# Optimization experiments

Measured on AMD Instinct MI355X. Metric: run time of the kernel, lower is better.

Reference implementation:

```python
import jax, jax.numpy as jnp
import numpy as np

N = 100000
E = 1000000
IN_C, HID, OUT_C = 128, 128, 40
DROPOUT_P = 0.5
BN_EPS = 1e-5


def setup_inputs() -> dict:
    key = jax.random.key(0)
    ks = jax.random.split(key, 10)
    x = jax.random.normal(ks[0], (N, IN_C), dtype=jnp.float32)
    edge_index = jax.random.randint(ks[1], (2, E), 0, N, dtype=jnp.int32)

    def glorot(k, fan_in, fan_out):
        lim = np.sqrt(6.0 / (fan_in + fan_out)).astype(np.float32)
        return jax.random.uniform(k, (fan_in, fan_out), jnp.float32, -lim, lim)

    return {
        "x": x,
        "edge_index": edge_index,
        "W1": glorot(ks[2], IN_C, HID), "b1": jnp.zeros((HID,), jnp.float32),
        "g1": jnp.ones((HID,), jnp.float32), "be1": jnp.zeros((HID,), jnp.float32),
        "W2": glorot(ks[3], HID, HID), "b2": jnp.zeros((HID,), jnp.float32),
        "g2": jnp.ones((HID,), jnp.float32), "be2": jnp.zeros((HID,), jnp.float32),
        "W3": glorot(ks[4], HID, OUT_C), "b3": jnp.zeros((OUT_C,), jnp.float32),
    }


def _deg_inv_sqrt(dst):
    # degree from destination nodes, +1 for the added self loop (PyG gcn_norm)
    deg = jax.ops.segment_sum(jnp.ones((E,), jnp.float32), dst, num_segments=N) + 1.0
    return jax.lax.rsqrt(deg)


def _gcn_conv(h, W, b, src, dst, dinv):
    # h: [N, Cin] -> [N, Cout]; y = D^-1/2 (A + I) D^-1/2 (h W) + b
    hw = h @ W
    norm = dinv[src] * dinv[dst]                      # [E]
    msg = hw[src] * norm[:, None]                     # [E, Cout] gather (memory-bound)
    agg = jax.ops.segment_sum(msg, dst, num_segments=N)
    agg = agg + hw * (dinv * dinv)[:, None]           # self-loop contribution
    return agg + b


def _batchnorm(h, gamma, beta):
    mu = jnp.mean(h, axis=0)
    var = jnp.mean(jnp.square(h - mu), axis=0)        # biased, training mode
    return (h - mu) * jax.lax.rsqrt(var + BN_EPS) * gamma + beta


def _dropout(h, key):
    keep = jax.random.bernoulli(key, 1.0 - DROPOUT_P, h.shape)
    return jnp.where(keep, h / (1.0 - DROPOUT_P), 0.0)


def reference(x, edge_index, W1, b1, g1, be1, W2, b2, g2, be2, W3, b3):
    src, dst = edge_index[0], edge_index[1]
    dinv = _deg_inv_sqrt(dst)
    dk = jax.random.split(jax.random.key(42), 2)

    h = _gcn_conv(x, W1, b1, src, dst, dinv)
    h = _dropout(jax.nn.relu(_batchnorm(h, g1, be1)), dk[0])

    h = _gcn_conv(h, W2, b2, src, dst, dinv)
    h = _dropout(jax.nn.relu(_batchnorm(h, g2, be2)), dk[1])

    h = _gcn_conv(h, W3, b3, src, dst, dinv)
    return jax.nn.log_softmax(h, axis=1)
```

## Files before the change

### kernel.cpp

```cpp
#include <hip/hip_runtime.h>
#include <math.h>

typedef __attribute__((ext_vector_type(8))) short bf16x8;
typedef __attribute__((ext_vector_type(4))) float f32x4;

__device__ __forceinline__ float bfbits2f(unsigned short b){
  return __uint_as_float(((unsigned)b) << 16);
}
__device__ __forceinline__ unsigned short f2bfbits(float f){
  unsigned u = __float_as_uint(f);
  unsigned r = u + 0x7fffu + ((u >> 16) & 1u);
  return (unsigned short)(r >> 16);
}

__device__ __forceinline__ uint4 ld16(const void* __restrict__ base, unsigned byteoff){
  return *(const uint4*)((const char*)base + byteoff);
}
__device__ __forceinline__ uint2 ld8(const void* __restrict__ base, unsigned byteoff){
  return *(const uint2*)((const char*)base + byteoff);
}

__host__ __device__ __forceinline__ unsigned rotl32(unsigned v, int d){
  return (v << d) | (v >> (32 - d));
}
__host__ __device__ __forceinline__ void tf2x32(unsigned k0, unsigned k1,
                                                unsigned c0, unsigned c1,
                                                unsigned &o0, unsigned &o1)
{
  unsigned ks2 = k0 ^ k1 ^ 0x1BD11BDAu;
  unsigned x0 = c0 + k0, x1 = c1 + k1;
#define TFR(r) x0 += x1; x1 = rotl32(x1, r); x1 ^= x0;
  TFR(13) TFR(15) TFR(26) TFR(6)
  x0 += k1;  x1 += ks2 + 1u;
  TFR(17) TFR(29) TFR(16) TFR(24)
  x0 += ks2; x1 += k0 + 2u;
  TFR(13) TFR(15) TFR(26) TFR(6)
  x0 += k0;  x1 += k1 + 3u;
  TFR(17) TFR(29) TFR(16) TFR(24)
  x0 += k1;  x1 += ks2 + 4u;
  TFR(13) TFR(15) TFR(26) TFR(6)
  x0 += ks2; x1 += k0 + 5u;
#undef TFR
  o0 = x0; o1 = x1;
}

__global__ __launch_bounds__(256) void k_countpos(const int* __restrict__ dst,
                                                  int* __restrict__ cnt,
                                                  int* __restrict__ pos, int E)
{
  int g = blockIdx.x * 256 + threadIdx.x;
  int base = g * 4;
  if (base + 3 < E){
    int4 d = ((const int4*)dst)[g];
    int4 p;
    p.x = atomicAdd(&cnt[d.x], 1);
    p.y = atomicAdd(&cnt[d.y], 1);
    p.z = atomicAdd(&cnt[d.z], 1);
    p.w = atomicAdd(&cnt[d.w], 1);
    ((int4*)pos)[g] = p;
  } else {
    for (int j = 0; j < 4; j++){
      int e = base + j;
      if (e < E) pos[e] = atomicAdd(&cnt[dst[e]], 1);
    }
  }
}

__global__ __launch_bounds__(256) void k_blocksum(const int* __restrict__ cnt,
                                                  int* __restrict__ bsum, int N)
{
  __shared__ int sh[256];
  int t = threadIdx.x;
  int base = blockIdx.x * 1024 + t * 4;
  int s = 0;
  #pragma unroll
  for (int j = 0; j < 4; j++){ int i = base + j; if (i < N) s += cnt[i]; }
  sh[t] = s; __syncthreads();
  for (int off = 128; off; off >>= 1){
    if (t < off) sh[t] += sh[t + off];
    __syncthreads();
  }
  if (t == 0) bsum[blockIdx.x] = sh[0];
}

__global__ __launch_bounds__(256) void k_scansums(const int* __restrict__ bsum,
                                                  int* __restrict__ boff,
                                                  int* __restrict__ rowstart,
                                                  int NB, int N)
{
  __shared__ int sh[256];
  int t = threadIdx.x;
  int v = (t < NB) ? bsum[t] : 0;
  sh[t] = v; __syncthreads();
  for (int off = 1; off < 256; off <<= 1){
    int x = sh[t];
    int y = (t >= off) ? sh[t - off] : 0;
    __syncthreads();
    sh[t] = x + y;
    __syncthreads();
  }
  if (t < NB) boff[t] = sh[t] - v;
  if (t == NB - 1) rowstart[N] = sh[t];
}

__global__ __launch_bounds__(256) void k_scanfinal(const int* __restrict__ cnt,
                                                   const int* __restrict__ boff,
                                                   int* __restrict__ rowstart,
                                                   float* __restrict__ dinv, int N)
{
  __shared__ int sh[256];
  int t = threadIdx.x;
  int base = blockIdx.x * 1024 + t * 4;
  int c0 = 0, c1 = 0, c2 = 0, c3 = 0;
  if (base + 0 < N) c0 = cnt[base + 0];
  if (base + 1 < N) c1 = cnt[base + 1];
  if (base + 2 < N) c2 = cnt[base + 2];
  if (base + 3 < N) c3 = cnt[base + 3];
  int s = c0 + c1 + c2 + c3;
  sh[t] = s; __syncthreads();
  for (int off = 1; off < 256; off <<= 1){
    int x = sh[t];
    int y = (t >= off) ? sh[t - off] : 0;
    __syncthreads();
    sh[t] = x + y;
    __syncthreads();
  }
  int excl = sh[t] - s + boff[blockIdx.x];
  if (base + 0 < N){ rowstart[base+0] = excl;          dinv[base+0] = rsqrtf((float)c0 + 1.f); }
  if (base + 1 < N){ rowstart[base+1] = excl+c0;       dinv[base+1] = rsqrtf((float)c1 + 1.f); }
  if (base + 2 < N){ rowstart[base+2] = excl+c0+c1;    dinv[base+2] = rsqrtf((float)c2 + 1.f); }
  if (base + 3 < N){ rowstart[base+3] = excl+c0+c1+c2; dinv[base+3] = rsqrtf((float)c3 + 1.f); }
}

__global__ __launch_bounds__(256) void k_fill(const int* __restrict__ src,
                                              const int* __restrict__ dst,
                                              const int* __restrict__ pos,
                                              const int* __restrict__ rowstart,
                                              int* __restrict__ csr, int E)
{
  int g = blockIdx.x * 256 + threadIdx.x;
  int base = g * 4;
  if (base + 3 < E){
    int4 d = ((const int4*)dst)[g];
    int4 p = ((const int4*)pos)[g];
    int4 s = ((const int4*)src)[g];
    int r0 = rowstart[d.x], r1 = rowstart[d.y], r2 = rowstart[d.z], r3 = rowstart[d.w];
    csr[r0 + p.x] = s.x;
    csr[r1 + p.y] = s.y;
    csr[r2 + p.z] = s.z;
    csr[r3 + p.w] = s.w;
  } else {
    for (int j = 0; j < 4; j++){
      int e = base + j;
      if (e < E) csr[rowstart[dst[e]] + pos[e]] = src[e];
    }
  }
}

__global__ __launch_bounds__(256) void k_wt(const float* __restrict__ W1,
                                            const float* __restrict__ W2,
                                            const float* __restrict__ W3,
                                            unsigned short* __restrict__ WT1,
                                            unsigned short* __restrict__ WT2,
                                            unsigned short* __restrict__ WT3)
{
  const float* W; unsigned short* WT; int Cout, Cpad;
  if (blockIdx.x == 0){ W = W1; WT = WT1; Cout = 128; Cpad = 128; }
  else if (blockIdx.x == 1){ W = W2; WT = WT2; Cout = 128; Cpad = 128; }
  else { W = W3; WT = WT3; Cout = 40; Cpad = 48; }
  int tot = Cpad * 128;
  for (int i = threadIdx.x; i < tot; i += 256){
    int n = i >> 7, k = i & 127;
    float v = (n < Cout) ? W[k * Cout + n] : 0.f;
    WT[i] = f2bfbits(v);
  }
}

template<int NT, int MODE, int MASKGEN>
__global__ __launch_bounds__(256) void k_gemm_mfma(const void* __restrict__ Ap,
                                                   const unsigned short* __restrict__ WT,
                                                   const float* __restrict__ dinv,
                                                   const float* __restrict__ stats,
                                                   const float* __restrict__ g,
                                                   const float* __restrict__ be,
                                                   const unsigned* __restrict__ mask,
                                                   unsigned* __restrict__ maskw,
                                                   unsigned wk0, unsigned wk1, int Mw,
                                                   float invN,
                                                   unsigned short* __restrict__ outb,
                                                   int N, int Cout, int Cstride)
{
  __shared__ uint4 Wl4[NT * 16 * 16];
  __shared__ float bnS[128], bnB[128];
  const int t = threadIdx.x;
  const int w = t >> 6, l = t & 63;
  const int lm = l & 15, q = l >> 4;
  const long rb0 = (long)blockIdx.x * 64;
  const int wrow0 = w * 16;
  const long grow = rb0 + wrow0 + lm;
  const bool inr = (grow < N);

  uint4 rawU[4];
  float4 rawF[4][2];
  uint4 mws;
  if (inr){
    #pragma unroll
    for (int kt = 0; kt < 4; kt++){
      int c = kt * 4 + q;
      if (MODE == 0){
        const float* ap = (const float*)Ap + grow * 128 + c * 8;
        rawF[kt][0] = *(const float4*)ap;
        rawF[kt][1] = *(const float4*)(ap + 4);
      } else {
        rawU[kt] = *(const uint4*)((const unsigned short*)Ap + grow * 128 + c * 8);
      }
    }
    if (MODE == 2) mws = *(const uint4*)(mask + ((unsigned)grow << 2));
  }

  {
    const uint4* s4 = (const uint4*)WT;
    const int tot = NT * 16 * 16;
    for (int i = t; i < tot; i += 256){
      int n = i >> 4, c = i & 15;
      Wl4[n * 16 + (c ^ (n & 15))] = s4[i];
    }
  }
  if (MODE == 2 && t < 128){
    float ss = 0.f, qq = 0.f;
    #pragma unroll
    for (int i = 0; i < 16; i++){
      ss += stats[i * 256 + t];
      qq += stats[i * 256 + 128 + t];
    }
    float mean = ss * invN;
    float var = fmaxf(qq * invN - mean * mean, 0.f);
    float rstd = rsqrtf(var + 1e-5f);
    float sc = g[t] * rstd;
    bnS[t] = sc;
    bnB[t] = be[t] - mean * sc;
  }
  __syncthreads();

  bf16x8 afr[4];
  #pragma unroll
  for (int kt = 0; kt < 4; kt++){
    uint4 chunk = make_uint4(0u, 0u, 0u, 0u);
    if (inr){
      if (MODE == 0){
        chunk.x = (unsigned)f2bfbits(rawF[kt][0].x) | ((unsigned)f2bfbits(rawF[kt][0].y) << 16);
        chunk.y = (unsigned)f2bfbits(rawF[kt][0].z) | ((unsigned)f2bfbits(rawF[kt][0].w) << 16);
        chunk.z = (unsigned)f2bfbits(rawF[kt][1].x) | ((unsigned)f2bfbits(rawF[kt][1].y) << 16);
        chunk.w = (unsigned)f2bfbits(rawF[kt][1].z) | ((unsigned)f2bfbits(rawF[kt][1].w) << 16);
      } else {
        int c = kt * 4 + q;
        unsigned mb = (&mws.x)[kt] >> (q * 8);
        const unsigned* rw = &rawU[kt].x;
        unsigned* cw = &chunk.x;
        #pragma unroll
        for (int h = 0; h < 4; h++){
          int ch = c * 8 + 2 * h;
          float f0 = bfbits2f((unsigned short)(rw[h] & 0xffffu));
          float f1 = bfbits2f((unsigned short)(rw[h] >> 16));
          f0 = fmaxf(fmaf(f0, bnS[ch],     bnB[ch]),     0.f);
          f1 = fmaxf(fmaf(f1, bnS[ch + 1], bnB[ch + 1]), 0.f);
          f0 = ((mb >> (2 * h))     & 1u) ? 0.f : f0 * 2.f;
          f1 = ((mb >> (2 * h + 1)) & 1u) ? 0.f : f1 * 2.f;
          cw[h] = (unsigned)f2bfbits(f0) | ((unsigned)f2bfbits(f1) << 16);
        }
      }
    }
    afr[kt] = *(bf16x8*)&chunk;
  }

  f32x4 acc[NT];
  #pragma unroll
  for (int nt = 0; nt < NT; nt++){
    acc[nt][0] = 0.f; acc[nt][1] = 0.f; acc[nt][2] = 0.f; acc[nt][3] = 0.f;
  }

  #pragma unroll
  for (int kt = 0; kt < 4; kt++){
    const int x = kt * 4 + q;
    #pragma unroll
    for (int nt = 0; nt < NT; nt++){
      int brow = nt * 16 + lm;
      bf16x8 b = *(const bf16x8*)&Wl4[brow * 16 + (x ^ (brow & 15))];
      acc[nt] = __builtin_amdgcn_mfma_f32_16x16x32_bf16(afr[kt], b, acc[nt], 0, 0, 0);
    }
  }

  #pragma unroll
  for (int r = 0; r < 4; r++){
    long row = rb0 + wrow0 + q * 4 + r;
    if (row < N){
      float dv = dinv[row];
      #pragma unroll
      for (int nt = 0; nt < NT; nt++){
        int col = nt * 16 + lm;
        if (col < Cout)
          outb[row * Cstride + col] = f2bfbits(acc[nt][r] * dv);
      }
    }
  }

  if (MASKGEN){
    int gg = blockIdx.x * 256 + t;
    if (gg < Mw){
      unsigned bits = 0u;
      #pragma unroll 4
      for (int j = 0; j < 32; j++){
        unsigned w0, w1;
        tf2x32(wk0, wk1, 0u, (unsigned)gg * 32u + (unsigned)j, w0, w1);
        bits |= (((w0 ^ w1) >> 31) << j);
      }
      maskw[gg] = bits;
    }
  }
}

#define ACC8(U) do{ uint4 _u = (U); \
  a0 += __uint_as_float(_u.x << 16); \
  a1 += __uint_as_float(_u.x & 0xffff0000u); \
  a2 += __uint_as_float(_u.y << 16); \
  a3 += __uint_as_float(_u.y & 0xffff0000u); \
  a4 += __uint_as_float(_u.z << 16); \
  a5 += __uint_as_float(_u.z & 0xffff0000u); \
  a6 += __uint_as_float(_u.w << 16); \
  a7 += __uint_as_float(_u.w & 0xffff0000u); }while(0)

__global__ __launch_bounds__(256) void k_agg128s(const unsigned short* __restrict__ hw,
                                                 const int* __restrict__ rs,
                                                 const int* __restrict__ csr,
                                                 const float* __restrict__ dinv,
                                                 unsigned short* __restrict__ outb,
                                                 float* __restrict__ stats,
                                                 int N)
{
  const int l = threadIdx.x;
  const int ns = l >> 4;
  const int sl = l & 15;
  const int ty = threadIdx.y;
  const int grp = ty * 4 + ns;
  const int base = blockIdx.x * 32;
  const unsigned slB = (unsigned)sl * 16u;

  float s0=0.f,s1=0.f,s2=0.f,s3=0.f,s4=0.f,s5=0.f,s6=0.f,s7=0.f;
  float q0=0.f,q1=0.f,q2=0.f,q3=0.f,q4=0.f,q5=0.f,q6=0.f,q7=0.f;

  #pragma unroll 1
  for (int it = 0; it < 2; it++){
    int v = base + it * 16 + grp;
    if (v < N){
      float a0=0.f,a1=0.f,a2=0.f,a3=0.f,a4=0.f,a5=0.f,a6=0.f,a7=0.f;
      ACC8(ld16(hw, (unsigned)v * 256u + slB));
      int e0 = rs[v], e1 = rs[v + 1];
      int i = e0;
      for (; i + 4 <= e1; i += 4){
        int sa = csr[i], sb = csr[i+1], sc = csr[i+2], sd = csr[i+3];
        uint4 m0 = ld16(hw, (unsigned)sa * 256u + slB);
        uint4 m1 = ld16(hw, (unsigned)sb * 256u + slB);
        uint4 m2 = ld16(hw, (unsigned)sc * 256u + slB);
        uint4 m3 = ld16(hw, (unsigned)sd * 256u + slB);
        ACC8(m0); ACC8(m1); ACC8(m2); ACC8(m3);
      }
      for (; i < e1; i++){
        ACC8(ld16(hw, (unsigned)csr[i] * 256u + slB));
      }
      float dv = dinv[v];
      a0*=dv; a1*=dv; a2*=dv; a3*=dv; a4*=dv; a5*=dv; a6*=dv; a7*=dv;
      uint4 o;
      o.x = (unsigned)f2bfbits(a0) | ((unsigned)f2bfbits(a1) << 16);
      o.y = (unsigned)f2bfbits(a2) | ((unsigned)f2bfbits(a3) << 16);
      o.z = (unsigned)f2bfbits(a4) | ((unsigned)f2bfbits(a5) << 16);
      o.w = (unsigned)f2bfbits(a6) | ((unsigned)f2bfbits(a7) << 16);
      *(uint4*)((char*)outb + (unsigned)v * 256u + slB) = o;
      s0+=a0; q0=fmaf(a0,a0,q0);  s1+=a1; q1=fmaf(a1,a1,q1);
      s2+=a2; q2=fmaf(a2,a2,q2);  s3+=a3; q3=fmaf(a3,a3,q3);
      s4+=a4; q4=fmaf(a4,a4,q4);  s5+=a5; q5=fmaf(a5,a5,q5);
      s6+=a6; q6=fmaf(a6,a6,q6);  s7+=a7; q7=fmaf(a7,a7,q7);
    }
  }

  __shared__ float shS[16][128], shQ[16][128];
  *(float4*)&shS[grp][sl * 8]     = make_float4(s0, s1, s2, s3);
  *(float4*)&shS[grp][sl * 8 + 4] = make_float4(s4, s5, s6, s7);
  *(float4*)&shQ[grp][sl * 8]     = make_float4(q0, q1, q2, q3);
  *(float4*)&shQ[grp][sl * 8 + 4] = make_float4(q4, q5, q6, q7);
  __syncthreads();
  int t = ty * 64 + threadIdx.x;
  if (t < 128){
    float ss = 0.f, qq = 0.f;
    #pragma unroll
    for (int g2 = 0; g2 < 16; g2++){ ss += shS[g2][t]; qq += shQ[g2][t]; }
    float* dstat = stats + (blockIdx.x & 15) * 256;
    atomicAdd(&dstat[t], ss);
    atomicAdd(&dstat[128 + t], qq);
  }
}

__global__ __launch_bounds__(256) void k_agg40lsm(const unsigned short* __restrict__ hw,
                                                  const int* __restrict__ rs,
                                                  const int* __restrict__ csr,
                                                  const float* __restrict__ dinv,
                                                  const float* __restrict__ b3,
                                                  float* __restrict__ out, int N)
{
  const int l = threadIdx.x;
  const int ns = l >> 4, sl = l & 15;
  const int v = blockIdx.x * 16 + threadIdx.y * 4 + ns;
  const bool act = (v < N) && (sl < 10);
  const unsigned slB = (unsigned)sl * 8u;
  float a0 = 0.f, a1 = 0.f, a2 = 0.f, a3 = 0.f, dv = 1.f;
  if (act){
    dv = dinv[v];
    uint2 u = ld8(hw, (unsigned)v * 128u + slB);
    a0 = __uint_as_float(u.x << 16);
    a1 = __uint_as_float(u.x & 0xffff0000u);
    a2 = __uint_as_float(u.y << 16);
    a3 = __uint_as_float(u.y & 0xffff0000u);
    int e0 = rs[v], e1 = rs[v + 1];
    int i = e0;
#define ACCU2(U) do{ uint2 _u = (U); \
    a0 += __uint_as_float(_u.x << 16); \
    a1 += __uint_as_float(_u.x & 0xffff0000u); \
    a2 += __uint_as_float(_u.y << 16); \
    a3 += __uint_as_float(_u.y & 0xffff0000u); }while(0)
    for (; i + 4 <= e1; i += 4){
      int sa = csr[i], sb = csr[i+1], sc = csr[i+2], sd = csr[i+3];
      uint2 m0 = ld8(hw, (unsigned)sa * 128u + slB);
      uint2 m1 = ld8(hw, (unsigned)sb * 128u + slB);
      uint2 m2 = ld8(hw, (unsigned)sc * 128u + slB);
      uint2 m3 = ld8(hw, (unsigned)sd * 128u + slB);
      ACCU2(m0); ACCU2(m1); ACCU2(m2); ACCU2(m3);
    }
    for (; i < e1; i++){
      ACCU2(ld8(hw, (unsigned)csr[i] * 128u + slB));
    }
#undef ACCU2
  }
  float x0 = act ? fmaf(a0, dv, b3[sl * 4 + 0]) : -INFINITY;
  float x1 = act ? fmaf(a1, dv, b3[sl * 4 + 1]) : -INFINITY;
  float x2 = act ? fmaf(a2, dv, b3[sl * 4 + 2]) : -INFINITY;
  float x3 = act ? fmaf(a3, dv, b3[sl * 4 + 3]) : -INFINITY;
  float m = fmaxf(fmaxf(x0, x1), fmaxf(x2, x3));
  #pragma unroll
  for (int off = 8; off; off >>= 1) m = fmaxf(m, __shfl_xor(m, off, 16));
  float e = act ? (expf(x0 - m) + expf(x1 - m) + expf(x2 - m) + expf(x3 - m)) : 0.f;
  #pragma unroll
  for (int off = 8; off; off >>= 1) e += __shfl_xor(e, off, 16);
  float lse = m + logf(e);
  if (act){
    float4 o;
    o.x = x0 - lse; o.y = x1 - lse; o.z = x2 - lse; o.w = x3 - lse;
    *reinterpret_cast<float4*>(out + (size_t)v * 40 + sl * 4) = o;
  }
}

extern "C" void kernel_launch(void* const* d_in, const int* in_sizes, int n_in,
                              void* d_out, int out_size, void* d_ws, size_t ws_size,
                              hipStream_t stream)
{
  const float* x  = (const float*)d_in[0];
  const int* ei   = (const int*)d_in[1];
  const float* W1 = (const float*)d_in[2];
  const float* g1 = (const float*)d_in[4];
  const float* be1= (const float*)d_in[5];
  const float* W2 = (const float*)d_in[6];
  const float* g2 = (const float*)d_in[8];
  const float* be2= (const float*)d_in[9];
  const float* W3 = (const float*)d_in[10];
  const float* b3 = (const float*)d_in[11];
  float* out = (float*)d_out;

  const int N = in_sizes[0] / 128;
  const int E = in_sizes[1] / 2;
  const int* srcv = ei;
  const int* dstv = ei + E;

  char* ws = (char*)d_ws;
  size_t off = 0;
  auto take = [&](size_t bytes) -> void* {
    void* p = ws + off;
    off = (off + bytes + 255) & ~(size_t)255;
    return p;
  };
  int*   cnt      = (int*)  take((size_t)N * 4);
  int*   pos      = (int*)  take((size_t)E * 4);
  int*   rowstart = (int*)  take((size_t)(N + 1) * 4);
  int*   csr      = (int*)  take((size_t)E * 4);
  float* dinv     = (float*)take((size_t)N * 4);
  int*   bsum     = (int*)  take(256 * 4);
  int*   boff     = (int*)  take(256 * 4);
  float* stats1   = (float*)take(2 * 16 * 256 * 4);
  float* stats2   = stats1 + 16 * 256;
  unsigned* mask1 = (unsigned*)take((size_t)N * 4 * 4);
  unsigned* mask2 = (unsigned*)take((size_t)N * 4 * 4);
  unsigned short* WT1 = (unsigned short*)take(128 * 128 * 2);
  unsigned short* WT2 = (unsigned short*)take(128 * 128 * 2);
  unsigned short* WT3 = (unsigned short*)take(48 * 128 * 2);
  unsigned short* bufX = (unsigned short*)take((size_t)N * 128 * 2);
  unsigned short* bufY = (unsigned short*)take((size_t)N * 128 * 2);
  (void)ws_size; (void)n_in; (void)out_size;

  unsigned l1k0, l1k1, l2k0, l2k1;
  tf2x32(0u, 42u, 0u, 0u, l1k0, l1k1);
  tf2x32(0u, 42u, 0u, 1u, l2k0, l2k1);

  const float invN = 1.0f / (float)N;
  const int M = N * 4;
  const int NB = (N + 1023) / 1024;
  dim3 wblk(64, 4);
  dim3 wgrid16((N + 15) / 16);
  dim3 wgrid32((N + 31) / 32);
  const int ggrid = (N + 63) / 64;
  const int egrid = (E + 1023) / 1024;

  hipMemsetAsync(cnt, 0, (size_t)N * 4, stream);
  hipMemsetAsync(stats1, 0, 2 * 16 * 256 * 4, stream);
  k_countpos<<<egrid, 256, 0, stream>>>(dstv, cnt, pos, E);
  k_blocksum<<<NB, 256, 0, stream>>>(cnt, bsum, N);
  k_scansums<<<1, 256, 0, stream>>>(bsum, boff, rowstart, NB, N);
  k_scanfinal<<<NB, 256, 0, stream>>>(cnt, boff, rowstart, dinv, N);
  k_fill<<<egrid, 256, 0, stream>>>(srcv, dstv, pos, rowstart, csr, E);
  k_wt<<<3, 256, 0, stream>>>(W1, W2, W3, WT1, WT2, WT3);

  k_gemm_mfma<8, 0, 1><<<ggrid, 256, 0, stream>>>(x, WT1, dinv,
      nullptr, nullptr, nullptr, nullptr, mask1, l1k0, l1k1, M,
      invN, bufX, N, 128, 128);
  k_agg128s<<<wgrid32, wblk, 0, stream>>>(bufX, rowstart, csr, dinv, bufY, stats1, N);

  k_gemm_mfma<8, 2, 1><<<ggrid, 256, 0, stream>>>(bufY, WT2, dinv,
      stats1, g1, be1, mask1, mask2, l2k0, l2k1, M,
      invN, bufX, N, 128, 128);
  k_agg128s<<<wgrid32, wblk, 0, stream>>>(bufX, rowstart, csr, dinv, bufY, stats2, N);

  k_gemm_mfma<3, 2, 0><<<ggrid, 256, 0, stream>>>(bufY, WT3, dinv,
      stats2, g2, be2, mask2, nullptr, 0u, 0u, 0,
      invN, bufX, N, 40, 64);
  k_agg40lsm<<<wgrid16, wblk, 0, stream>>>(bufX, rowstart, csr, dinv, b3, out, N);
}
```

Measured before the change: 423.9 us.

## Merge setup kernels: fused init/zero, single-pass scan, GEMM1 with CSR fill

Replaces the two memsets and the weight-transpose kernel with one init kernel that also zeroes the counters and stats. The block-sum scan is folded into each final-scan block by redundantly scanning the block sums. The first GEMM and the CSR fill run as one launch with disjoint block ranges. Together this drops several launches and serial gaps, at the cost of uneven block roles and shared-memory sizing driven by the GEMM path.

```diff
diff --git a/kernel.cpp b/kernel.cpp
--- a/kernel.cpp
+++ b/kernel.cpp
@@ -44,6 +44,31 @@
   o0 = x0; o1 = x1;
 }
 
+__global__ __launch_bounds__(256) void k_init(const float* __restrict__ W1,
+                                              const float* __restrict__ W2,
+                                              const float* __restrict__ W3,
+                                              unsigned short* __restrict__ WT1,
+                                              unsigned short* __restrict__ WT2,
+                                              unsigned short* __restrict__ WT3,
+                                              uint4* __restrict__ zbase, int zwords)
+{
+  if (blockIdx.x < 3){
+    const float* W; unsigned short* WT; int Cout, Cpad;
+    if (blockIdx.x == 0){ W = W1; WT = WT1; Cout = 128; Cpad = 128; }
+    else if (blockIdx.x == 1){ W = W2; WT = WT2; Cout = 128; Cpad = 128; }
+    else { W = W3; WT = WT3; Cout = 40; Cpad = 48; }
+    int tot = Cpad * 128;
+    for (int i = threadIdx.x; i < tot; i += 256){
+      int n = i >> 7, k = i & 127;
+      float v = (n < Cout) ? W[k * Cout + n] : 0.f;
+      WT[i] = f2bfbits(v);
+    }
+  } else {
+    int idx = (blockIdx.x - 3) * 256 + threadIdx.x;
+    if (idx < zwords) zbase[idx] = make_uint4(0u, 0u, 0u, 0u);
+  }
+}
+
 __global__ __launch_bounds__(256) void k_countpos(const int* __restrict__ dst,
                                                   int* __restrict__ cnt,
                                                   int* __restrict__ pos, int E)
@@ -83,15 +108,16 @@
   if (t == 0) bsum[blockIdx.x] = sh[0];
 }
 
-__global__ __launch_bounds__(256) void k_scansums(const int* __restrict__ bsum,
-                                                  int* __restrict__ boff,
-                                                  int* __restrict__ rowstart,
-                                                  int NB, int N)
+__global__ __launch_bounds__(256) void k_scanfinal(const int* __restrict__ cnt,
+                                                   const int* __restrict__ bsum,
+                                                   int* __restrict__ rowstart,
+                                                   float* __restrict__ dinv,
+                                                   int NB, int N)
 {
   __shared__ int sh[256];
   int t = threadIdx.x;
-  int v = (t < NB) ? bsum[t] : 0;
-  sh[t] = v; __syncthreads();
+  int vb = (t < NB) ? bsum[t] : 0;
+  sh[t] = vb; __syncthreads();
   for (int off = 1; off < 256; off <<= 1){
     int x = sh[t];
     int y = (t >= off) ? sh[t - off] : 0;
@@ -99,17 +125,9 @@
     sh[t] = x + y;
     __syncthreads();
   }
-  if (t < NB) boff[t] = sh[t] - v;
-  if (t == NB - 1) rowstart[N] = sh[t];
-}
-
-__global__ __launch_bounds__(256) void k_scanfinal(const int* __restrict__ cnt,
-                                                   const int* __restrict__ boff,
-                                                   int* __restrict__ rowstart,
-                                                   float* __restrict__ dinv, int N)
-{
-  __shared__ int sh[256];
-  int t = threadIdx.x;
+  if (blockIdx.x == 0 && t == 0) rowstart[N] = sh[NB - 1];
+  int boffb = sh[blockIdx.x] - bsum[blockIdx.x];
+  __syncthreads();
   int base = blockIdx.x * 1024 + t * 4;
   int c0 = 0, c1 = 0, c2 = 0, c3 = 0;
   if (base + 0 < N) c0 = cnt[base + 0];
@@ -125,20 +143,21 @@
     sh[t] = x + y;
     __syncthreads();
   }
-  int excl = sh[t] - s + boff[blockIdx.x];
+  int excl = sh[t] - s + boffb;
   if (base + 0 < N){ rowstart[base+0] = excl;          dinv[base+0] = rsqrtf((float)c0 + 1.f); }
   if (base + 1 < N){ rowstart[base+1] = excl+c0;       dinv[base+1] = rsqrtf((float)c1 + 1.f); }
   if (base + 2 < N){ rowstart[base+2] = excl+c0+c1;    dinv[base+2] = rsqrtf((float)c2 + 1.f); }
   if (base + 3 < N){ rowstart[base+3] = excl+c0+c1+c2; dinv[base+3] = rsqrtf((float)c3 + 1.f); }
 }
 
-__global__ __launch_bounds__(256) void k_fill(const int* __restrict__ src,
-                                              const int* __restrict__ dst,
-                                              const int* __restrict__ pos,
-                                              const int* __restrict__ rowstart,
-                                              int* __restrict__ csr, int E)
-{
-  int g = blockIdx.x * 256 + threadIdx.x;
+__device__ __forceinline__ void fill_body(int bid,
+                                          const int* __restrict__ src,
+                                          const int* __restrict__ dst,
+                                          const int* __restrict__ pos,
+                                          const int* __restrict__ rowstart,
+                                          int* __restrict__ csr, int E)
+{
+  int g = bid * 256 + threadIdx.x;
   int base = g * 4;
   if (base + 3 < E){
     int4 d = ((const int4*)dst)[g];
@@ -157,45 +176,27 @@
   }
 }
 
-__global__ __launch_bounds__(256) void k_wt(const float* __restrict__ W1,
-                                            const float* __restrict__ W2,
-                                            const float* __restrict__ W3,
-                                            unsigned short* __restrict__ WT1,
-                                            unsigned short* __restrict__ WT2,
-                                            unsigned short* __restrict__ WT3)
-{
-  const float* W; unsigned short* WT; int Cout, Cpad;
-  if (blockIdx.x == 0){ W = W1; WT = WT1; Cout = 128; Cpad = 128; }
-  else if (blockIdx.x == 1){ W = W2; WT = WT2; Cout = 128; Cpad = 128; }
-  else { W = W3; WT = WT3; Cout = 40; Cpad = 48; }
-  int tot = Cpad * 128;
-  for (int i = threadIdx.x; i < tot; i += 256){
-    int n = i >> 7, k = i & 127;
-    float v = (n < Cout) ? W[k * Cout + n] : 0.f;
-    WT[i] = f2bfbits(v);
-  }
-}
-
 template<int NT, int MODE, int MASKGEN>
-__global__ __launch_bounds__(256) void k_gemm_mfma(const void* __restrict__ Ap,
-                                                   const unsigned short* __restrict__ WT,
-                                                   const float* __restrict__ dinv,
-                                                   const float* __restrict__ stats,
-                                                   const float* __restrict__ g,
-                                                   const float* __restrict__ be,
-                                                   const unsigned* __restrict__ mask,
-                                                   unsigned* __restrict__ maskw,
-                                                   unsigned wk0, unsigned wk1, int Mw,
-                                                   float invN,
-                                                   unsigned short* __restrict__ outb,
-                                                   int N, int Cout, int Cstride)
+__device__ __forceinline__ void gemm_body(int bid,
+                                          const void* __restrict__ Ap,
+                                          const unsigned short* __restrict__ WT,
+                                          const float* __restrict__ dinv,
+                                          const float* __restrict__ stats,
+                                          const float* __restrict__ g,
+                                          const float* __restrict__ be,
+                                          const unsigned* __restrict__ mask,
+                                          unsigned* __restrict__ maskw,
+                                          unsigned wk0, unsigned wk1, int Mw,
+                                          float invN,
+                                          unsigned short* __restrict__ outb,
+                                          int N, int Cout, int Cstride)
 {
   __shared__ uint4 Wl4[NT * 16 * 16];
   __shared__ float bnS[128], bnB[128];
   const int t = threadIdx.x;
   const int w = t >> 6, l = t & 63;
   const int lm = l & 15, q = l >> 4;
-  const long rb0 = (long)blockIdx.x * 64;
+  const long rb0 = (long)bid * 64;
   const int wrow0 = w * 16;
   const long grow = rb0 + wrow0 + lm;
   const bool inr = (grow < N);
@@ -305,7 +306,7 @@
   }
 
   if (MASKGEN){
-    int gg = blockIdx.x * 256 + t;
+    int gg = bid * 256 + t;
     if (gg < Mw){
       unsigned bits = 0u;
       #pragma unroll 4
@@ -317,6 +318,44 @@
       maskw[gg] = bits;
     }
   }
+}
+
+__global__ __launch_bounds__(256) void k_g1f(const void* __restrict__ Ap,
+                                             const unsigned short* __restrict__ WT,
+                                             const float* __restrict__ dinv,
+                                             unsigned* __restrict__ maskw,
+                                             unsigned wk0, unsigned wk1, int Mw,
+                                             unsigned short* __restrict__ outb, int N,
+                                             const int* __restrict__ src,
+                                             const int* __restrict__ dst,
+                                             const int* __restrict__ pos,
+                                             const int* __restrict__ rowstart,
+                                             int* __restrict__ csr, int E, int gg)
+{
+  if ((int)blockIdx.x < gg){
+    gemm_body<8, 0, 1>(blockIdx.x, Ap, WT, dinv, nullptr, nullptr, nullptr,
+                       nullptr, maskw, wk0, wk1, Mw, 0.f, outb, N, 128, 128);
+  } else {
+    fill_body(blockIdx.x - gg, src, dst, pos, rowstart, csr, E);
+  }
+}
+
+template<int NT, int MODE, int MASKGEN>
+__global__ __launch_bounds__(256) void k_gemm_mfma(const void* __restrict__ Ap,
+                                                   const unsigned short* __restrict__ WT,
+                                                   const float* __restrict__ dinv,
+                                                   const float* __restrict__ stats,
+                                                   const float* __restrict__ g,
+                                                   const float* __restrict__ be,
+                                                   const unsigned* __restrict__ mask,
+                                                   unsigned* __restrict__ maskw,
+                                                   unsigned wk0, unsigned wk1, int Mw,
+                                                   float invN,
+                                                   unsigned short* __restrict__ outb,
+                                                   int N, int Cout, int Cstride)
+{
+  gemm_body<NT, MODE, MASKGEN>(blockIdx.x, Ap, WT, dinv, stats, g, be, mask,
+                               maskw, wk0, wk1, Mw, invN, outb, N, Cout, Cstride);
 }
 
 #define ACC8(U) do{ uint4 _u = (U); \
@@ -486,14 +525,14 @@
     return p;
   };
   int*   cnt      = (int*)  take((size_t)N * 4);
+  float* stats1   = (float*)take(2 * 16 * 256 * 4);
+  float* stats2   = stats1 + 16 * 256;
+  size_t zlen = off;
   int*   pos      = (int*)  take((size_t)E * 4);
   int*   rowstart = (int*)  take((size_t)(N + 1) * 4);
   int*   csr      = (int*)  take((size_t)E * 4);
   float* dinv     = (float*)take((size_t)N * 4);
   int*   bsum     = (int*)  take(256 * 4);
-  int*   boff     = (int*)  take(256 * 4);
-  float* stats1   = (float*)take(2 * 16 * 256 * 4);
-  float* stats2   = stats1 + 16 * 256;
   unsigned* mask1 = (unsigned*)take((size_t)N * 4 * 4);
   unsigned* mask2 = (unsigned*)take((size_t)N * 4 * 4);
   unsigned short* WT1 = (unsigned short*)take(128 * 128 * 2);
@@ -515,19 +554,16 @@
   dim3 wgrid32((N + 31) / 32);
   const int ggrid = (N + 63) / 64;
   const int egrid = (E + 1023) / 1024;
-
-  hipMemsetAsync(cnt, 0, (size_t)N * 4, stream);
-  hipMemsetAsync(stats1, 0, 2 * 16 * 256 * 4, stream);
+  const int zwords = (int)(zlen / 16);
+  const int zgrid = 3 + (zwords + 255) / 256;
+
+  k_init<<<zgrid, 256, 0, stream>>>(W1, W2, W3, WT1, WT2, WT3, (uint4*)cnt, zwords);
   k_countpos<<<egrid, 256, 0, stream>>>(dstv, cnt, pos, E);
   k_blocksum<<<NB, 256, 0, stream>>>(cnt, bsum, N);
-  k_scansums<<<1, 256, 0, stream>>>(bsum, boff, rowstart, NB, N);
-  k_scanfinal<<<NB, 256, 0, stream>>>(cnt, boff, rowstart, dinv, N);
-  k_fill<<<egrid, 256, 0, stream>>>(srcv, dstv, pos, rowstart, csr, E);
-  k_wt<<<3, 256, 0, stream>>>(W1, W2, W3, WT1, WT2, WT3);
-
-  k_gemm_mfma<8, 0, 1><<<ggrid, 256, 0, stream>>>(x, WT1, dinv,
-      nullptr, nullptr, nullptr, nullptr, mask1, l1k0, l1k1, M,
-      invN, bufX, N, 128, 128);
+  k_scanfinal<<<NB, 256, 0, stream>>>(cnt, bsum, rowstart, dinv, NB, N);
+
+  k_g1f<<<ggrid + egrid, 256, 0, stream>>>(x, WT1, dinv, mask1, l1k0, l1k1, M,
+      bufX, N, srcv, dstv, pos, rowstart, csr, E, ggrid);
   k_agg128s<<<wgrid32, wblk, 0, stream>>>(bufX, rowstart, csr, dinv, bufY, stats1, N);
 
   k_gemm_mfma<8, 2, 1><<<ggrid, 256, 0, stream>>>(bufY, WT2, dinv,
```

New measurement: 399.7 us. 1.06x faster.
